# Performance work log

Hardware: AMD Instinct MI355X
Metric: run time of the kernel (lower is better)

## Reference

```python
import jax, jax.numpy as jnp
import numpy as np

ADJ_SIZE = 512
START_POS = 128
END_POS = 384
IN_FEATURES = 128
OUT_FEATURES = 128
BATCH = 64
BN_EPS = 1e-5


def setup_inputs() -> dict:
    key = jax.random.key(0)
    k1, k2, k3 = jax.random.split(key, 3)
    inputs = {
        "input": jax.random.normal(k1, (BATCH, ADJ_SIZE, IN_FEATURES), dtype=jnp.float32),
        "adj": jax.random.uniform(k2, (BATCH, ADJ_SIZE, ADJ_SIZE), dtype=jnp.float32),
        "weight": jax.random.normal(k3, (IN_FEATURES, OUT_FEATURES), dtype=jnp.float32) * (1.0 / np.sqrt(IN_FEATURES)),
        "gamma": jnp.ones((OUT_FEATURES * ADJ_SIZE,), dtype=jnp.float32),
        "beta": jnp.zeros((OUT_FEATURES * ADJ_SIZE,), dtype=jnp.float32),
    }
    return inputs


def _crop_mask(n, s, e, dtype):
    # zeros everywhere except the [s:e, s:e] crop block, set to 1
    idx = jnp.arange(n)
    in_crop = (idx >= s) & (idx < e)
    return (in_crop[:, None] & in_crop[None, :]).astype(dtype)  # [N, N]


def reference(input, adj, weight, gamma, beta):
    B, N, _ = input.shape
    # support = input @ weight : [B, N, F_out]
    support = jnp.einsum('bni,io->bno', input, weight)
    # mask adjacency to the crop block
    mask = _crop_mask(N, START_POS, END_POS, adj.dtype)
    adj_ = adj * mask  # [B, N, N]
    # aggregated output : [B, N, F_out]
    output_ = jnp.einsum('bnm,bmf->bnf', adj_, support)
    F = output_.shape[2]
    # BatchNorm1d over flattened (N * F) features, training-mode batch stats
    x = output_.reshape(B, N * F)
    mean = jnp.mean(x, axis=0)
    var = jnp.mean(jnp.square(x - mean), axis=0)  # biased variance (torch BN)
    x_hat = (x - mean) * jax.lax.rsqrt(var + BN_EPS)
    y = x_hat * gamma + beta
    return y.reshape(B, N, F)
```

## Files before the change

### kernel.cpp

```cpp
#include <hip/hip_runtime.h>
#include <hip/hip_bf16.h>

#define BATCH 64
#define NADJ  512
#define F     128
#define CROP0 128
#define CROP1 384
#define CN    256
#define BN_EPS 1e-5f

typedef __attribute__((ext_vector_type(8))) short short8;
typedef __attribute__((ext_vector_type(4))) float f32x4;

__device__ __forceinline__ ushort f2bf(float x) {
  __hip_bfloat16 h = __float2bfloat16(x);
  return *reinterpret_cast<ushort*>(&h);
}

__device__ __forceinline__ short8 cvt8(const float4 a, const float4 b) {
  short8 r;
  r[0] = (short)f2bf(a.x); r[1] = (short)f2bf(a.y);
  r[2] = (short)f2bf(a.z); r[3] = (short)f2bf(a.w);
  r[4] = (short)f2bf(b.x); r[5] = (short)f2bf(b.y);
  r[6] = (short)f2bf(b.z); r[7] = (short)f2bf(b.w);
  return r;
}

__global__ __launch_bounds__(512, 1) void gcn_ka(
    const float* __restrict__ input, const float* __restrict__ adj,
    const float* __restrict__ W, const float* __restrict__ beta,
    float* __restrict__ out, float* __restrict__ Ocrop) {
  const int x = blockIdx.x & 7, y = blockIdx.x >> 3;
  const int b  = ((y >> 2) << 3) | x;
  const int qt = y & 3;
  __shared__ ushort wt[128][136];
  __shared__ ushort ain[64][136];
  __shared__ ushort stl[128][268];
  const int tid = threadIdx.x;
  const int l = tid & 63, w = tid >> 6;
  const int lr = l & 15, lg = l >> 4;

  const int n0  = qt * 64 + (w & 3) * 16;
  const int wf0 = (w >> 2) * 64;
  const float* a0 =
      adj + ((size_t)b * NADJ + CROP0 + n0 + lr) * NADJ + CROP0;
  float4 xreg[16];
#pragma unroll
  for (int ks = 0; ks < 8; ++ks) {
    const int k0 = ks * 32 + lg * 8;
    xreg[2 * ks]     = *reinterpret_cast<const float4*>(&a0[k0]);
    xreg[2 * ks + 1] = *reinterpret_cast<const float4*>(&a0[k0 + 4]);
  }

  {
    const int gid = blockIdx.x * 512 + tid;
#pragma unroll
    for (int q = 0; q < 4; ++q) {
      const int g2 = gid + q * 131072;
      const int c4 = (g2 & 31) * 4;
      const int rr = (g2 >> 5) & 255;
      const int bb = g2 >> 13;
      const int n  = rr < 128 ? rr : rr + 256;
      const float4 bv =
          *reinterpret_cast<const float4*>(&beta[(size_t)n * F + c4]);
      *reinterpret_cast<float4*>(&out[((size_t)bb * NADJ + n) * F + c4]) = bv;
    }
  }

  {
    const int i0 = tid & 63;
    const int fq = (tid >> 6) * 16;
#pragma unroll
    for (int ih = 0; ih < 2; ++ih) {
      const int i = i0 + ih * 64;
      const float* wr = &W[(size_t)i * F + fq];
      float4 v[4];
#pragma unroll
      for (int q = 0; q < 4; ++q)
        v[q] = reinterpret_cast<const float4*>(wr)[q];
#pragma unroll
      for (int q = 0; q < 4; ++q) {
        wt[fq + q * 4 + 0][i] = f2bf(v[q].x);
        wt[fq + q * 4 + 1][i] = f2bf(v[q].y);
        wt[fq + q * 4 + 2][i] = f2bf(v[q].z);
        wt[fq + q * 4 + 3][i] = f2bf(v[q].w);
      }
    }
  }

  const float* inb = input + ((size_t)b * NADJ + CROP0) * F;
  const int msub = (w & 3) * 16;
  const int sf0  = (w >> 2) * 64;
  const int ml0  = tid >> 5;
  const int ic4  = (tid & 31) * 4;
  float4 pv[4];
#pragma unroll
  for (int q = 0; q < 4; ++q)
    pv[q] = *reinterpret_cast<const float4*>(
        &inb[(size_t)(ml0 + q * 16) * F + ic4]);

  for (int mc = 0; mc < CN; mc += 64) {
#pragma unroll
    for (int q = 0; q < 4; ++q)
      *reinterpret_cast<ushort4*>(&ain[ml0 + q * 16][ic4]) =
          make_ushort4(f2bf(pv[q].x), f2bf(pv[q].y), f2bf(pv[q].z),
                       f2bf(pv[q].w));
    __syncthreads();
    if (mc + 64 < CN) {
#pragma unroll
      for (int q = 0; q < 4; ++q)
        pv[q] = *reinterpret_cast<const float4*>(
            &inb[(size_t)(mc + 64 + ml0 + q * 16) * F + ic4]);
    }
    f32x4 sacc[4] = {};
#pragma unroll
    for (int ks = 0; ks < 4; ++ks) {
      const int k0 = ks * 32 + lg * 8;
      const short8 av = *reinterpret_cast<const short8*>(&ain[msub + lr][k0]);
#pragma unroll
      for (int fi = 0; fi < 4; ++fi) {
        const short8 bv =
            *reinterpret_cast<const short8*>(&wt[sf0 + fi * 16 + lr][k0]);
        sacc[fi] =
            __builtin_amdgcn_mfma_f32_16x16x32_bf16(av, bv, sacc[fi], 0, 0, 0);
      }
    }
#pragma unroll
    for (int fi = 0; fi < 4; ++fi)
      *reinterpret_cast<ushort4*>(
          &stl[sf0 + fi * 16 + lr][mc + msub + lg * 4]) =
          make_ushort4(f2bf(sacc[fi][0]), f2bf(sacc[fi][1]),
                       f2bf(sacc[fi][2]), f2bf(sacc[fi][3]));
    __syncthreads();
  }

  f32x4 acc[4] = {};
#pragma unroll
  for (int ks = 0; ks < 8; ++ks) {
    const int k0 = ks * 32 + lg * 8;
    const short8 av = cvt8(xreg[2 * ks], xreg[2 * ks + 1]);
#pragma unroll
    for (int fi = 0; fi < 4; ++fi) {
      const short8 bv =
          *reinterpret_cast<const short8*>(&stl[wf0 + fi * 16 + lr][k0]);
      acc[fi] =
          __builtin_amdgcn_mfma_f32_16x16x32_bf16(av, bv, acc[fi], 0, 0, 0);
    }
  }
#pragma unroll
  for (int fi = 0; fi < 4; ++fi) {
    const int f = wf0 + fi * 16 + lr;
    const int n = n0 + lg * 4;
#pragma unroll
    for (int r = 0; r < 4; ++r)
      Ocrop[((size_t)b * CN + n + r) * F + f] = acc[fi][r];
  }
}

__global__ __launch_bounds__(256) void gcn_kb(
    const float* __restrict__ Ocrop, float* __restrict__ out,
    const float* __restrict__ gamma, const float* __restrict__ beta) {
  __shared__ float s_l[256], s2_l[256], m_l[64], r_l[64];
  const int tid = threadIdx.x;
  const int jl = tid & 63, bg = tid >> 6;
  const int j  = blockIdx.x * 64 + jl;
  const int nl = j >> 7, f = j & 127;
  const int nf = (CROP0 + nl) * F + f;
  const float* p = Ocrop + (size_t)j + (size_t)bg * 16 * CN * F;

  float x[16];
  float s = 0.f, s2 = 0.f;
#pragma unroll
  for (int bb = 0; bb < 16; ++bb) {
    x[bb] = p[(size_t)bb * CN * F];
    s += x[bb];
    s2 += x[bb] * x[bb];
  }
  s_l[tid]  = s;
  s2_l[tid] = s2;
  __syncthreads();
  if (tid < 64) {
    s  = s_l[jl] + s_l[64 + jl] + s_l[128 + jl] + s_l[192 + jl];
    s2 = s2_l[jl] + s2_l[64 + jl] + s2_l[128 + jl] + s2_l[192 + jl];
    const float mean = s * (1.f / BATCH);
    const float var  = s2 * (1.f / BATCH) - mean * mean;
    m_l[jl] = mean;
    r_l[jl] = rsqrtf(var + BN_EPS);
  }
  __syncthreads();
  const float mean = m_l[jl];
  const float a    = r_l[jl] * gamma[nf];
  const float c    = beta[nf] - mean * a;
#pragma unroll
  for (int bb = 0; bb < 16; ++bb)
    out[(size_t)nf + (size_t)(bg * 16 + bb) * NADJ * F] = x[bb] * a + c;
}

extern "C" void kernel_launch(void* const* d_in, const int* in_sizes, int n_in,
                              void* d_out, int out_size, void* d_ws,
                              size_t ws_size, hipStream_t stream) {
  const float* input = (const float*)d_in[0];
  const float* adj   = (const float*)d_in[1];
  const float* W     = (const float*)d_in[2];
  const float* gamma = (const float*)d_in[3];
  const float* beta  = (const float*)d_in[4];
  float* out = (float*)d_out;

  float* Ocrop = (float*)d_ws;

  gcn_ka<<<256, 512, 0, stream>>>(input, adj, W, beta, out, Ocrop);
  gcn_kb<<<512, 256, 0, stream>>>(Ocrop, out, gamma, beta);
}
```

Measured before the change: 25.13 us.

## Split feature dimension across blocks to double grid size in gcn_ka

Each gcn_ka block now computes only half of the output features (64 instead of 128), doubling the grid to 512 blocks and halving shared memory per block so up to 4 blocks can co-reside. The adjacency row prefetch is split into two halves, with the second half loaded after the support GEMM to reduce register pressure. This raises parallelism on a 256-CU device at the cost of recomputing part of the work: each block re-reads the input/adj tiles and redoes the conversion for its feature half.

```diff
diff --git a/kernel.cpp b/kernel.cpp
--- a/kernel.cpp
+++ b/kernel.cpp
@@ -26,37 +26,38 @@
   return r;
 }
 
-__global__ __launch_bounds__(512, 1) void gcn_ka(
+__global__ __launch_bounds__(512, 4) void gcn_ka(
     const float* __restrict__ input, const float* __restrict__ adj,
     const float* __restrict__ W, const float* __restrict__ beta,
     float* __restrict__ out, float* __restrict__ Ocrop) {
   const int x = blockIdx.x & 7, y = blockIdx.x >> 3;
-  const int b  = ((y >> 2) << 3) | x;
-  const int qt = y & 3;
-  __shared__ ushort wt[128][136];
+  const int b   = ((y >> 3) << 3) | x;
+  const int sub = y & 7;
+  const int fh  = sub >> 2;
+  const int qt  = sub & 3;
+  __shared__ ushort wt[64][136];
   __shared__ ushort ain[64][136];
-  __shared__ ushort stl[128][268];
+  __shared__ ushort stl[64][268];
   const int tid = threadIdx.x;
   const int l = tid & 63, w = tid >> 6;
   const int lr = l & 15, lg = l >> 4;
 
   const int n0  = qt * 64 + (w & 3) * 16;
-  const int wf0 = (w >> 2) * 64;
   const float* a0 =
       adj + ((size_t)b * NADJ + CROP0 + n0 + lr) * NADJ + CROP0;
-  float4 xreg[16];
-#pragma unroll
-  for (int ks = 0; ks < 8; ++ks) {
+  float4 xregA[8];
+#pragma unroll
+  for (int ks = 0; ks < 4; ++ks) {
     const int k0 = ks * 32 + lg * 8;
-    xreg[2 * ks]     = *reinterpret_cast<const float4*>(&a0[k0]);
-    xreg[2 * ks + 1] = *reinterpret_cast<const float4*>(&a0[k0 + 4]);
+    xregA[2 * ks]     = *reinterpret_cast<const float4*>(&a0[k0]);
+    xregA[2 * ks + 1] = *reinterpret_cast<const float4*>(&a0[k0 + 4]);
   }
 
   {
     const int gid = blockIdx.x * 512 + tid;
 #pragma unroll
-    for (int q = 0; q < 4; ++q) {
-      const int g2 = gid + q * 131072;
+    for (int q = 0; q < 2; ++q) {
+      const int g2 = gid + q * 262144;
       const int c4 = (g2 & 31) * 4;
       const int rr = (g2 >> 5) & 255;
       const int bb = g2 >> 13;
@@ -68,29 +69,25 @@
   }
 
   {
-    const int i0 = tid & 63;
-    const int fq = (tid >> 6) * 16;
-#pragma unroll
-    for (int ih = 0; ih < 2; ++ih) {
-      const int i = i0 + ih * 64;
-      const float* wr = &W[(size_t)i * F + fq];
-      float4 v[4];
-#pragma unroll
-      for (int q = 0; q < 4; ++q)
-        v[q] = reinterpret_cast<const float4*>(wr)[q];
-#pragma unroll
-      for (int q = 0; q < 4; ++q) {
-        wt[fq + q * 4 + 0][i] = f2bf(v[q].x);
-        wt[fq + q * 4 + 1][i] = f2bf(v[q].y);
-        wt[fq + q * 4 + 2][i] = f2bf(v[q].z);
-        wt[fq + q * 4 + 3][i] = f2bf(v[q].w);
-      }
+    const int i  = tid & 127;
+    const int fg = (tid >> 7) * 16;
+    const float* wr = &W[(size_t)i * F + fh * 64 + fg];
+    float4 v[4];
+#pragma unroll
+    for (int q = 0; q < 4; ++q)
+      v[q] = reinterpret_cast<const float4*>(wr)[q];
+#pragma unroll
+    for (int q = 0; q < 4; ++q) {
+      wt[fg + q * 4 + 0][i] = f2bf(v[q].x);
+      wt[fg + q * 4 + 1][i] = f2bf(v[q].y);
+      wt[fg + q * 4 + 2][i] = f2bf(v[q].z);
+      wt[fg + q * 4 + 3][i] = f2bf(v[q].w);
     }
   }
 
   const float* inb = input + ((size_t)b * NADJ + CROP0) * F;
   const int msub = (w & 3) * 16;
-  const int sf0  = (w >> 2) * 64;
+  const int sfq  = (w >> 2) * 32;
   const int ml0  = tid >> 5;
   const int ic4  = (tid & 31) * 4;
   float4 pv[4];
@@ -112,44 +109,53 @@
         pv[q] = *reinterpret_cast<const float4*>(
             &inb[(size_t)(mc + 64 + ml0 + q * 16) * F + ic4]);
     }
-    f32x4 sacc[4] = {};
+    f32x4 sacc[2] = {};
 #pragma unroll
     for (int ks = 0; ks < 4; ++ks) {
       const int k0 = ks * 32 + lg * 8;
       const short8 av = *reinterpret_cast<const short8*>(&ain[msub + lr][k0]);
 #pragma unroll
-      for (int fi = 0; fi < 4; ++fi) {
+      for (int fi = 0; fi < 2; ++fi) {
         const short8 bv =
-            *reinterpret_cast<const short8*>(&wt[sf0 + fi * 16 + lr][k0]);
+            *reinterpret_cast<const short8*>(&wt[sfq + fi * 16 + lr][k0]);
         sacc[fi] =
             __builtin_amdgcn_mfma_f32_16x16x32_bf16(av, bv, sacc[fi], 0, 0, 0);
       }
     }
 #pragma unroll
-    for (int fi = 0; fi < 4; ++fi)
+    for (int fi = 0; fi < 2; ++fi)
       *reinterpret_cast<ushort4*>(
-          &stl[sf0 + fi * 16 + lr][mc + msub + lg * 4]) =
+          &stl[sfq + fi * 16 + lr][mc + msub + lg * 4]) =
           make_ushort4(f2bf(sacc[fi][0]), f2bf(sacc[fi][1]),
                        f2bf(sacc[fi][2]), f2bf(sacc[fi][3]));
     __syncthreads();
   }
 
-  f32x4 acc[4] = {};
+  float4 xregB[8];
+#pragma unroll
+  for (int ks = 0; ks < 4; ++ks) {
+    const int k0 = 128 + ks * 32 + lg * 8;
+    xregB[2 * ks]     = *reinterpret_cast<const float4*>(&a0[k0]);
+    xregB[2 * ks + 1] = *reinterpret_cast<const float4*>(&a0[k0 + 4]);
+  }
+  f32x4 acc[2] = {};
 #pragma unroll
   for (int ks = 0; ks < 8; ++ks) {
     const int k0 = ks * 32 + lg * 8;
-    const short8 av = cvt8(xreg[2 * ks], xreg[2 * ks + 1]);
-#pragma unroll
-    for (int fi = 0; fi < 4; ++fi) {
+    const short8 av = (ks < 4)
+                          ? cvt8(xregA[2 * ks], xregA[2 * ks + 1])
+                          : cvt8(xregB[2 * (ks - 4)], xregB[2 * (ks - 4) + 1]);
+#pragma unroll
+    for (int fi = 0; fi < 2; ++fi) {
       const short8 bv =
-          *reinterpret_cast<const short8*>(&stl[wf0 + fi * 16 + lr][k0]);
+          *reinterpret_cast<const short8*>(&stl[sfq + fi * 16 + lr][k0]);
       acc[fi] =
           __builtin_amdgcn_mfma_f32_16x16x32_bf16(av, bv, acc[fi], 0, 0, 0);
     }
   }
 #pragma unroll
-  for (int fi = 0; fi < 4; ++fi) {
-    const int f = wf0 + fi * 16 + lr;
+  for (int fi = 0; fi < 2; ++fi) {
+    const int f = fh * 64 + sfq + fi * 16 + lr;
     const int n = n0 + lg * 4;
 #pragma unroll
     for (int r = 0; r < 4; ++r)
@@ -208,6 +214,6 @@
 
   float* Ocrop = (float*)d_ws;
 
-  gcn_ka<<<256, 512, 0, stream>>>(input, adj, W, beta, out, Ocrop);
+  gcn_ka<<<512, 512, 0, stream>>>(input, adj, W, beta, out, Ocrop);
   gcn_kb<<<512, 256, 0, stream>>>(Ocrop, out, gamma, beta);
 }
```

After: 26.55 us. 1.06x slower.

## Interleave aggregation MFMAs with support chunks and store intermediate as bf16

Applied to the files above, without the earlier changes.

The adj×support MFMAs for each completed 64-column chunk of support now run inside the support-computation loop, so they overlap with the next chunk's global loads instead of waiting for all four chunks. Separately, the cropped intermediate written between the two kernels is stored as bf16 rather than fp32, halving that workspace traffic, and the BN kernel widens it back to float. The bf16 rounding of the pre-normalization output adds precision error to the batch statistics, and the strided 2-byte loads in the second kernel may coalesce less well.

```diff
diff --git a/kernel.cpp b/kernel.cpp
--- a/kernel.cpp
+++ b/kernel.cpp
@@ -17,6 +17,13 @@
   return *reinterpret_cast<ushort*>(&h);
 }
 
+__device__ __forceinline__ float bf2f(ushort u) {
+  const unsigned v = (unsigned)u << 16;
+  float f;
+  __builtin_memcpy(&f, &v, 4);
+  return f;
+}
+
 __device__ __forceinline__ short8 cvt8(const float4 a, const float4 b) {
   short8 r;
   r[0] = (short)f2bf(a.x); r[1] = (short)f2bf(a.y);
@@ -29,7 +36,7 @@
 __global__ __launch_bounds__(512, 1) void gcn_ka(
     const float* __restrict__ input, const float* __restrict__ adj,
     const float* __restrict__ W, const float* __restrict__ beta,
-    float* __restrict__ out, float* __restrict__ Ocrop) {
+    float* __restrict__ out, ushort* __restrict__ Ocrop) {
   const int x = blockIdx.x & 7, y = blockIdx.x >> 3;
   const int b  = ((y >> 2) << 3) | x;
   const int qt = y & 3;
@@ -99,18 +106,37 @@
     pv[q] = *reinterpret_cast<const float4*>(
         &inb[(size_t)(ml0 + q * 16) * F + ic4]);
 
-  for (int mc = 0; mc < CN; mc += 64) {
+  f32x4 acc[4] = {};
+#pragma unroll
+  for (int cc = 0; cc < 4; ++cc) {
+    const int mc = cc * 64;
 #pragma unroll
     for (int q = 0; q < 4; ++q)
       *reinterpret_cast<ushort4*>(&ain[ml0 + q * 16][ic4]) =
           make_ushort4(f2bf(pv[q].x), f2bf(pv[q].y), f2bf(pv[q].z),
                        f2bf(pv[q].w));
     __syncthreads();
-    if (mc + 64 < CN) {
+    if (cc < 3) {
 #pragma unroll
       for (int q = 0; q < 4; ++q)
         pv[q] = *reinterpret_cast<const float4*>(
             &inb[(size_t)(mc + 64 + ml0 + q * 16) * F + ic4]);
+    }
+    if (cc > 0) {
+      const int kb0 = mc - 64;
+#pragma unroll
+      for (int ks2 = 0; ks2 < 2; ++ks2) {
+        const int ks = (cc - 1) * 2 + ks2;
+        const int k0 = kb0 + ks2 * 32 + lg * 8;
+        const short8 av = cvt8(xreg[2 * ks], xreg[2 * ks + 1]);
+#pragma unroll
+        for (int fi = 0; fi < 4; ++fi) {
+          const short8 bv =
+              *reinterpret_cast<const short8*>(&stl[wf0 + fi * 16 + lr][k0]);
+          acc[fi] =
+              __builtin_amdgcn_mfma_f32_16x16x32_bf16(av, bv, acc[fi], 0, 0, 0);
+        }
+      }
     }
     f32x4 sacc[4] = {};
 #pragma unroll
@@ -134,10 +160,10 @@
     __syncthreads();
   }
 
-  f32x4 acc[4] = {};
-#pragma unroll
-  for (int ks = 0; ks < 8; ++ks) {
-    const int k0 = ks * 32 + lg * 8;
+#pragma unroll
+  for (int ks2 = 0; ks2 < 2; ++ks2) {
+    const int ks = 6 + ks2;
+    const int k0 = 192 + ks2 * 32 + lg * 8;
     const short8 av = cvt8(xreg[2 * ks], xreg[2 * ks + 1]);
 #pragma unroll
     for (int fi = 0; fi < 4; ++fi) {
@@ -147,18 +173,19 @@
           __builtin_amdgcn_mfma_f32_16x16x32_bf16(av, bv, acc[fi], 0, 0, 0);
     }
   }
+
 #pragma unroll
   for (int fi = 0; fi < 4; ++fi) {
     const int f = wf0 + fi * 16 + lr;
     const int n = n0 + lg * 4;
 #pragma unroll
     for (int r = 0; r < 4; ++r)
-      Ocrop[((size_t)b * CN + n + r) * F + f] = acc[fi][r];
+      Ocrop[((size_t)b * CN + n + r) * F + f] = f2bf(acc[fi][r]);
   }
 }
 
 __global__ __launch_bounds__(256) void gcn_kb(
-    const float* __restrict__ Ocrop, float* __restrict__ out,
+    const ushort* __restrict__ Ocrop, float* __restrict__ out,
     const float* __restrict__ gamma, const float* __restrict__ beta) {
   __shared__ float s_l[256], s2_l[256], m_l[64], r_l[64];
   const int tid = threadIdx.x;
@@ -166,13 +193,13 @@
   const int j  = blockIdx.x * 64 + jl;
   const int nl = j >> 7, f = j & 127;
   const int nf = (CROP0 + nl) * F + f;
-  const float* p = Ocrop + (size_t)j + (size_t)bg * 16 * CN * F;
+  const ushort* p = Ocrop + (size_t)j + (size_t)bg * 16 * CN * F;
 
   float x[16];
   float s = 0.f, s2 = 0.f;
 #pragma unroll
   for (int bb = 0; bb < 16; ++bb) {
-    x[bb] = p[(size_t)bb * CN * F];
+    x[bb] = bf2f(p[(size_t)bb * CN * F]);
     s += x[bb];
     s2 += x[bb] * x[bb];
   }
@@ -206,7 +233,7 @@
   const float* beta  = (const float*)d_in[4];
   float* out = (float*)d_out;
 
-  float* Ocrop = (float*)d_ws;
+  ushort* Ocrop = (ushort*)d_ws;
 
   gcn_ka<<<256, 512, 0, stream>>>(input, adj, W, beta, out, Ocrop);
   gcn_kb<<<512, 256, 0, stream>>>(Ocrop, out, gamma, beta);
```

New measurement: 23.50 us. -6.5%, faster.
